# Kernel optimization log

Measured on AMD Instinct MI355X. Metric: run time of the kernel, lower is better.

Reference implementation:

```python
import jax, jax.numpy as jnp
import numpy as np

CUTOFF = 4.0
RBF_N = 32          # distance_embedding_size == D_rbf
F_DIM = 128         # hidden_size
N_ATOMS = 20000
N_PROBES = 100000
N_EDGES = 262144
LN_EPS = 1e-5


def setup_inputs() -> dict:
    key = jax.random.key(0)
    ks = jax.random.split(key, 20)
    s = 0.02
    inp = {
        "diff_pi": jax.random.normal(ks[0], (N_EDGES, 3), jnp.float32),
        "S_JK": jax.random.normal(ks[1], (N_ATOMS, F_DIM), jnp.float32),
        "V_JK": jax.random.normal(ks[2], (N_ATOMS, 3, F_DIM), jnp.float32),
        "atom_idx": jax.random.randint(ks[3], (N_EDGES,), 0, N_ATOMS),
        "probe_idx": jax.random.randint(ks[4], (N_EDGES,), 0, N_PROBES),
        "num_probes": N_PROBES,
        # state branch params
        "w_s1": jax.random.normal(ks[5], (3 * F_DIM, F_DIM), jnp.float32) * s,
        "b_s1": jnp.zeros((F_DIM,), jnp.float32),
        "g_ln": jnp.ones((F_DIM,), jnp.float32),
        "b_ln": jnp.zeros((F_DIM,), jnp.float32),
        "w_s2": jax.random.normal(ks[6], (F_DIM, F_DIM), jnp.float32) * s,
        "b_s2": jnp.zeros((F_DIM,), jnp.float32),
        # filter branch params
        "w_f1": jax.random.normal(ks[7], (RBF_N, F_DIM), jnp.float32) * s,
        "b_f1": jnp.zeros((F_DIM,), jnp.float32),
        "w_f2": jax.random.normal(ks[8], (F_DIM, F_DIM), jnp.float32) * s,
        "b_f2": jnp.zeros((F_DIM,), jnp.float32),
        # output head params
        "w_o1": jax.random.normal(ks[9], (F_DIM, F_DIM // 2), jnp.float32) * s,
        "b_o1": jnp.zeros((F_DIM // 2,), jnp.float32),
        "w_o2": jax.random.normal(ks[10], (F_DIM // 2, 1), jnp.float32) * s,
        "b_o2": jnp.zeros((1,), jnp.float32),
        "final_bias": jnp.array([-6.1], jnp.float32),
    }
    return inp


def reference(diff_pi, S_JK, V_JK, atom_idx, probe_idx, num_probes,
              w_s1, b_s1, g_ln, b_ln, w_s2, b_s2,
              w_f1, b_f1, w_f2, b_f2,
              w_o1, b_o1, w_o2, b_o2, final_bias):
    silu = jax.nn.silu
    # edge distances
    sq = (diff_pi ** 2).sum(-1)                       # [E]
    dist = jnp.sqrt(sq)                               # [E] exact distance
    dist_safe = jnp.sqrt(sq + 1e-8)[:, None]          # [E,1]
    r_hat = diff_pi / dist_safe                       # [E,3]

    # sinc RBF expansion: sin(n*pi*d/cutoff)/d, n=1..RBF_N
    n = jnp.arange(1, RBF_N + 1, dtype=diff_pi.dtype) # [D]
    e_pi = jnp.sin(dist[:, None] * n * (jnp.pi / CUTOFF)) / dist[:, None]  # [E,D]

    # gather atom features to edges
    n_i = jnp.sqrt((V_JK ** 2).sum(1) + 1e-8)         # [N,F]
    n_e = n_i[atom_idx]                               # [E,F]
    V_e = V_JK[atom_idx]                              # [E,3,F]
    q_pi = (V_e * r_hat[:, :, None]).sum(1)           # [E,F]
    S_e = S_JK[atom_idx]                              # [E,F]

    # state branch: Linear -> LayerNorm -> SiLU -> Linear
    h = jnp.concatenate([S_e, n_e, q_pi], axis=-1)    # [E,3F]
    u = h @ w_s1 + b_s1                               # [E,F]
    mu = u.mean(-1, keepdims=True)
    var = ((u - mu) ** 2).mean(-1, keepdims=True)
    u_norm = (u - mu) / jnp.sqrt(var + LN_EPS) * g_ln + b_ln
    state = silu(u_norm) @ w_s2 + b_s2                # [E,F]

    # filter branch (no normalization -> absolute distance scale)
    W = silu(e_pi @ w_f1 + b_f1) @ w_f2 + b_f2        # [E,F]

    # fuse + output head
    m = (silu((W * state) @ w_o1 + b_o1) @ w_o2 + b_o2)[:, 0]  # [E]

    x = dist / CUTOFF
    env = 1.0 - 21.0 * x ** 5 + 35.0 * x ** 6 - 15.0 * x ** 7
    env = jnp.where(dist < CUTOFF, env, jnp.zeros_like(env))
    m_w = m * env

    # scatter-add to probes
    rho = jax.ops.segment_sum(m_w, probe_idx, num_segments=num_probes)
    return rho + final_bias[0]
```

## Files before the change

kernel.cpp:

```cpp
#include <hip/hip_runtime.h>

#define EPB     64
#define E_TOTAL 262144
#define NPROBE  100000
#define N_ATOMS 20000
#define NTAB    2048

#define ASTR   136
#define A2_O   0
#define LDS_SH 8704

#define WS1_O  0
#define WS2_O  49152
#define WO1_O  65536
#define WT_TOT 73728
#define PQ_B   147456
#define WTI_B  20627456
#define WTF_B  21676032
#define CNT_B  22725120
#define CUR_B  22805120
#define SA_B   22885120
#define ED_B   23933696

typedef __attribute__((ext_vector_type(8))) short          short8;
typedef __attribute__((ext_vector_type(8))) unsigned short ushort8;
typedef __attribute__((ext_vector_type(4))) float          floatx4;

#define MFMA16(a, b, c) __builtin_amdgcn_mfma_f32_16x16x32_bf16((a), (b), (c), 0, 0, 0)

__device__ __forceinline__ unsigned short f2bfu(float x) {
    unsigned u = __builtin_bit_cast(unsigned, x);
    u = (u + 0x7FFFu + ((u >> 16) & 1u)) >> 16;
    return (unsigned short)u;
}
__device__ __forceinline__ unsigned pk2(float lo, float hi) {
    return __builtin_amdgcn_perm(__builtin_bit_cast(unsigned, hi),
                                 __builtin_bit_cast(unsigned, lo), 0x07060302u);
}
__device__ __forceinline__ float bf2f(unsigned short u) {
    return __builtin_bit_cast(float, ((unsigned)u) << 16);
}
__device__ __forceinline__ float silu_f(float x) { return x / (1.0f + __expf(-x)); }

struct F8 { float v[8]; };
__device__ __forceinline__ F8 ld8(const float* __restrict__ p) {
    F8 r;
    const float4 a = *(const float4*)p;
    const float4 b = *(const float4*)(p + 4);
    r.v[0] = a.x; r.v[1] = a.y; r.v[2] = a.z; r.v[3] = a.w;
    r.v[4] = b.x; r.v[5] = b.y; r.v[6] = b.z; r.v[7] = b.w;
    return r;
}

__global__ void cfr_prep_w(const float* __restrict__ w_s1, const float* __restrict__ w_s2,
                           const float* __restrict__ w_o1,
                           const float* __restrict__ fb, float* __restrict__ out,
                           unsigned short* __restrict__ wt, int* __restrict__ cnt) {
    int i = blockIdx.x * 256 + threadIdx.x;
    if (i < NPROBE) out[i] = fb[0];
    if (i < N_ATOMS) cnt[i] = 0;
    if (i < WT_TOT) {
        float v;
        if (i < WS2_O)      { int n = i / 384, k = i - n * 384;          v = w_s1[k * 128 + n]; }
        else if (i < WO1_O) { int j = i - WS2_O, n = j >> 7, k = j & 127; v = w_s2[k * 128 + n]; }
        else                { int j = i - WO1_O, n = j >> 7, k = j & 127; v = w_o1[k * 64 + n]; }
        wt[i] = f2bfu(v);
    }
}

__global__ void cfr_hist(const int* __restrict__ atom_idx, int* __restrict__ cnt) {
    int e = blockIdx.x * 256 + threadIdx.x;
    if (e < E_TOTAL) atomicAdd(&cnt[atom_idx[e]], 1);
}

__global__ __launch_bounds__(1024) void cfr_scan(const int* __restrict__ cnt,
                                                 int* __restrict__ cur) {
    __shared__ int part[1024];
    const int t = threadIdx.x, base = t * 20;
    int loc[20]; int s = 0;
#pragma unroll
    for (int i = 0; i < 20; ++i) {
        int v = (base + i < N_ATOMS) ? cnt[base + i] : 0;
        loc[i] = s; s += v;
    }
    part[t] = s;
    __syncthreads();
    for (int d = 1; d < 1024; d <<= 1) {
        int v = (t >= d) ? part[t - d] : 0;
        __syncthreads();
        part[t] += v;
        __syncthreads();
    }
    int pre = (t == 0) ? 0 : part[t - 1];
#pragma unroll
    for (int i = 0; i < 20; ++i)
        if (base + i < N_ATOMS) cur[base + i] = pre + loc[i];
}

__global__ void cfr_scatter(const int* __restrict__ atom_idx, const int* __restrict__ probe_idx,
                            const float* __restrict__ diff,
                            int* __restrict__ cur, int* __restrict__ sortedA,
                            float4* __restrict__ ediff) {
    int e = blockIdx.x * 256 + threadIdx.x;
    if (e >= E_TOTAL) return;
    int a = atom_idx[e];
    int pos = atomicAdd(&cur[a], 1);
    sortedA[pos] = a;
    float4 ed;
    ed.x = diff[e * 3 + 0]; ed.y = diff[e * 3 + 1]; ed.z = diff[e * 3 + 2];
    ed.w = __int_as_float(probe_idx[e]);
    ediff[pos] = ed;
}

__global__ __launch_bounds__(128) void cfr_prep_wtab(
    const float* __restrict__ w_f1, const float* __restrict__ b_f1,
    const float* __restrict__ w_f2, const float* __restrict__ b_f2,
    float* __restrict__ wtabF)
{
    __shared__ float ep[32];
    __shared__ float f1s[128];
    const int t = threadIdx.x, row = blockIdx.x;
    float d = fmaxf(row * (4.0f / NTAB), 1e-4f);
    if (t < 32) ep[t] = sinf(d * (t + 1) * 0.7853981633974483f) / d;
    __syncthreads();
    float f1 = b_f1[t];
#pragma unroll
    for (int k = 0; k < 32; ++k) f1 = fmaf(ep[k], w_f1[k * 128 + t], f1);
    f1s[t] = silu_f(f1);
    __syncthreads();
    float w = b_f2[t];
#pragma unroll 4
    for (int k = 0; k < 128; ++k) w = fmaf(f1s[k], w_f2[k * 128 + t], w);
    wtabF[row * 128 + t] = w;
}

__global__ void cfr_prep_wtab_pack(const float* __restrict__ wtabF,
                                   unsigned* __restrict__ wtabI) {
    int i = blockIdx.x * 256 + threadIdx.x;
    if (i >= NTAB * 128) return;
    int r = i >> 7, c = i & 127;
    unsigned lo = f2bfu(wtabF[r * 128 + c]);
    unsigned hi = f2bfu(wtabF[(r + 1) * 128 + c]);
    wtabI[i] = (hi << 16) | lo;
}

__global__ __launch_bounds__(256, 3) void cfr_prep_pq(
    const float* __restrict__ S, const float* __restrict__ V,
    const float* __restrict__ b_s1,
    const unsigned short* __restrict__ wt, unsigned short* __restrict__ pq)
{
    __shared__ __align__(16) unsigned short bufH[32 * 264];
    __shared__ __align__(16) unsigned short bufV[96 * 136];

    const int t    = threadIdx.x;
    const int a0   = blockIdx.x * 32;
    const int wave = t >> 6;
    const int lane = t & 63;
    const int q    = lane >> 4;
    const int c16  = lane & 15;

#pragma unroll
    for (int it = 0; it < 2; ++it) {
        int idx = it * 256 + t;
        int al = idx >> 4, f8 = (idx & 15) * 8;
        int a = a0 + al;
        ushort8 sS, sN, s0, s1, s2;
        if (a < N_ATOMS) {
            F8 s  = ld8(S + a * 128 + f8);
            F8 v0 = ld8(V + a * 384 + f8);
            F8 v1 = ld8(V + a * 384 + 128 + f8);
            F8 v2 = ld8(V + a * 384 + 256 + f8);
#pragma unroll
            for (int j = 0; j < 8; ++j) {
                sS[j] = f2bfu(s.v[j]);
                sN[j] = f2bfu(sqrtf(v0.v[j]*v0.v[j] + v1.v[j]*v1.v[j] + v2.v[j]*v2.v[j] + 1e-8f));
                s0[j] = f2bfu(v0.v[j]);
                s1[j] = f2bfu(v1.v[j]);
                s2[j] = f2bfu(v2.v[j]);
            }
        } else {
#pragma unroll
            for (int j = 0; j < 8; ++j) { sS[j]=0; sN[j]=0; s0[j]=0; s1[j]=0; s2[j]=0; }
        }
        *(ushort8*)&bufH[al * 264 + f8]        = sS;
        *(ushort8*)&bufH[al * 264 + 128 + f8]  = sN;
        *(ushort8*)&bufV[al * 136 + f8]        = s0;
        *(ushort8*)&bufV[(32 + al) * 136 + f8] = s1;
        *(ushort8*)&bufV[(64 + al) * 136 + f8] = s2;
    }
    __syncthreads();

    const floatx4 zero4 = {0.f, 0.f, 0.f, 0.f};
    float bs1c[2];
#pragma unroll
    for (int ni = 0; ni < 2; ++ni) bs1c[ni] = b_s1[wave * 32 + ni * 16 + c16];

    {
        floatx4 pacc[2][2];
#pragma unroll
        for (int mi = 0; mi < 2; ++mi) { pacc[mi][0] = zero4; pacc[mi][1] = zero4; }
#pragma unroll
        for (int kk = 0; kk < 8; ++kk) {
            short8 bfr[2], af[2];
#pragma unroll
            for (int ni = 0; ni < 2; ++ni) {
                int n = wave * 32 + ni * 16 + c16;
                bfr[ni] = *(const short8*)&wt[WS1_O + n * 384 + kk * 32 + q * 8];
            }
#pragma unroll
            for (int mi = 0; mi < 2; ++mi)
                af[mi] = *(const short8*)&bufH[(mi * 16 + c16) * 264 + kk * 32 + q * 8];
#pragma unroll
            for (int mi = 0; mi < 2; ++mi)
#pragma unroll
                for (int ni = 0; ni < 2; ++ni)
                    pacc[mi][ni] = MFMA16(af[mi], bfr[ni], pacc[mi][ni]);
        }
#pragma unroll
        for (int mi = 0; mi < 2; ++mi)
#pragma unroll
            for (int r = 0; r < 4; ++r) {
                int a = a0 + mi * 16 + q * 4 + r;
                if (a < N_ATOMS)
#pragma unroll
                    for (int ni = 0; ni < 2; ++ni) {
                        int col = wave * 32 + ni * 16 + c16;
                        pq[a * 512 + col] = f2bfu(pacc[mi][ni][r] + bs1c[ni]);
                    }
            }
    }

    short8 bq[4][2];
#pragma unroll
    for (int kk = 0; kk < 4; ++kk)
#pragma unroll
        for (int ni = 0; ni < 2; ++ni) {
            int n = wave * 32 + ni * 16 + c16;
            bq[kk][ni] = *(const short8*)&wt[WS1_O + n * 384 + 256 + kk * 32 + q * 8];
        }
#pragma unroll
    for (int d = 0; d < 3; ++d) {
        floatx4 qacc[2][2];
#pragma unroll
        for (int mi = 0; mi < 2; ++mi) { qacc[mi][0] = zero4; qacc[mi][1] = zero4; }
#pragma unroll
        for (int kk = 0; kk < 4; ++kk) {
            short8 af[2];
#pragma unroll
            for (int mi = 0; mi < 2; ++mi)
                af[mi] = *(const short8*)&bufV[(d * 32 + mi * 16 + c16) * 136 + kk * 32 + q * 8];
#pragma unroll
            for (int mi = 0; mi < 2; ++mi)
#pragma unroll
                for (int ni = 0; ni < 2; ++ni)
                    qacc[mi][ni] = MFMA16(af[mi], bq[kk][ni], qacc[mi][ni]);
        }
#pragma unroll
        for (int mi = 0; mi < 2; ++mi)
#pragma unroll
            for (int r = 0; r < 4; ++r) {
                int a = a0 + mi * 16 + q * 4 + r;
                if (a < N_ATOMS)
#pragma unroll
                    for (int ni = 0; ni < 2; ++ni) {
                        int col = wave * 32 + ni * 16 + c16;
                        pq[a * 512 + (1 + d) * 128 + col] = f2bfu(qacc[mi][ni][r]);
                    }
            }
    }
}

__global__ __launch_bounds__(256, 8) void cfr_main(
    const int* __restrict__ aidx, const float4* __restrict__ ediff,
    const unsigned short* __restrict__ wt, const unsigned short* __restrict__ pq,
    const unsigned* __restrict__ wtabI,
    const float* __restrict__ g_ln, const float* __restrict__ b_ln,
    const float* __restrict__ b_s2, const float* __restrict__ b_o1,
    const float* __restrict__ w_o2, const float* __restrict__ b_o2,
    float* __restrict__ out)
{
    __shared__ __align__(16) unsigned short LDSu[LDS_SH];
    __shared__ float df[EPB];
    __shared__ int   probe_s[EPB];
    __shared__ float mpart[EPB * 4];

    const int t    = threadIdx.x;
    const int e0   = blockIdx.x * EPB;
    const int wave = t >> 6;
    const int lane = t & 63;
    const int q    = lane >> 4;
    const int c16  = lane & 15;
    const floatx4 zero4 = {0.f, 0.f, 0.f, 0.f};

    const int el = t >> 2;
    const int c0 = (t & 3) * 32;

    {
        const int eg = e0 + el;
        const int a  = aidx[eg];
        float4 ed = ediff[eg];
        float sq = ed.x * ed.x + ed.y * ed.y + ed.z * ed.z;
        float dist = sqrtf(sq);
        float rinv = rsqrtf(sq + 1e-8f);
        float rx = ed.x * rinv, ry = ed.y * rinv, rz = ed.z * rinv;
        if ((t & 3) == 0) { df[el] = dist; probe_s[el] = __float_as_int(ed.w); }

        const ushort8* pqr = (const ushort8*)(pq + a * 512 + c0);
        float u[32];
#pragma unroll
        for (int g = 0; g < 4; ++g) {
            ushort8 v = pqr[g];
#pragma unroll
            for (int j = 0; j < 8; ++j) u[g * 8 + j] = bf2f(v[j]);
        }
#pragma unroll
        for (int g = 0; g < 4; ++g) {
            ushort8 v = pqr[16 + g];
#pragma unroll
            for (int j = 0; j < 8; ++j) u[g * 8 + j] = fmaf(bf2f(v[j]), rx, u[g * 8 + j]);
        }
#pragma unroll
        for (int g = 0; g < 4; ++g) {
            ushort8 v = pqr[32 + g];
#pragma unroll
            for (int j = 0; j < 8; ++j) u[g * 8 + j] = fmaf(bf2f(v[j]), ry, u[g * 8 + j]);
        }
#pragma unroll
        for (int g = 0; g < 4; ++g) {
            ushort8 v = pqr[48 + g];
#pragma unroll
            for (int j = 0; j < 8; ++j) u[g * 8 + j] = fmaf(bf2f(v[j]), rz, u[g * 8 + j]);
        }
        float s = 0.f, s2 = 0.f;
#pragma unroll
        for (int j = 0; j < 32; ++j) { s += u[j]; s2 = fmaf(u[j], u[j], s2); }
        s  += __shfl_xor(s, 1);  s  += __shfl_xor(s, 2);
        s2 += __shfl_xor(s2, 1); s2 += __shfl_xor(s2, 2);
        float mu = s * (1.f / 128.f);
        float rstd = rsqrtf(s2 * (1.f / 128.f) - mu * mu + 1e-5f);
        const float4* gp = (const float4*)(g_ln + c0);
        const float4* bp = (const float4*)(b_ln + c0);
        unsigned pko[16];
#pragma unroll
        for (int g4 = 0; g4 < 8; ++g4) {
            float4 gg = gp[g4], bb = bp[g4];
            float y0 = silu_f((u[g4 * 4 + 0] - mu) * rstd * gg.x + bb.x);
            float y1 = silu_f((u[g4 * 4 + 1] - mu) * rstd * gg.y + bb.y);
            float y2 = silu_f((u[g4 * 4 + 2] - mu) * rstd * gg.z + bb.z);
            float y3 = silu_f((u[g4 * 4 + 3] - mu) * rstd * gg.w + bb.w);
            pko[g4 * 2 + 0] = pk2(y0, y1);
            pko[g4 * 2 + 1] = pk2(y2, y3);
        }
        uint4* dst = (uint4*)&LDSu[A2_O + el * ASTR + c0];
        dst[0] = make_uint4(pko[0], pko[1], pko[2], pko[3]);
        dst[1] = make_uint4(pko[4], pko[5], pko[6], pko[7]);
        dst[2] = make_uint4(pko[8], pko[9], pko[10], pko[11]);
        dst[3] = make_uint4(pko[12], pko[13], pko[14], pko[15]);
    }
    __syncthreads();

    {
        floatx4 sacc[4][2];
#pragma unroll
        for (int mi = 0; mi < 4; ++mi) { sacc[mi][0] = zero4; sacc[mi][1] = zero4; }
#pragma unroll
        for (int kk = 0; kk < 4; ++kk) {
            short8 a2f[4], b2[2];
#pragma unroll
            for (int ni = 0; ni < 2; ++ni) {
                int n = wave * 32 + ni * 16 + c16;
                b2[ni] = *(const short8*)&wt[WS2_O + n * 128 + kk * 32 + q * 8];
            }
#pragma unroll
            for (int mi = 0; mi < 4; ++mi)
                a2f[mi] = *(const short8*)&LDSu[A2_O + (mi * 16 + c16) * ASTR + kk * 32 + q * 8];
#pragma unroll
            for (int mi = 0; mi < 4; ++mi)
#pragma unroll
                for (int ni = 0; ni < 2; ++ni)
                    sacc[mi][ni] = MFMA16(a2f[mi], b2[ni], sacc[mi][ni]);
        }
        __syncthreads();

        float bs2c[2];
#pragma unroll
        for (int ni = 0; ni < 2; ++ni) bs2c[ni] = b_s2[wave * 32 + ni * 16 + c16];
#pragma unroll
        for (int mi = 0; mi < 4; ++mi) {
#pragma unroll
            for (int r = 0; r < 4; ++r) {
                int row = mi * 16 + q * 4 + r;
                float f  = fminf(df[row] * (NTAB / 4.0f), NTAB - 1.01f);
                float fi = floorf(f);
                int   i0 = (int)fi;
                float fr = f - fi;
                const unsigned* wrow = wtabI + i0 * 128;
#pragma unroll
                for (int ni = 0; ni < 2; ++ni) {
                    int col = wave * 32 + ni * 16 + c16;
                    unsigned wp = wrow[col];
                    float w0 = __builtin_bit_cast(float, wp << 16);
                    float w1 = __builtin_bit_cast(float, wp & 0xffff0000u);
                    float wv = fmaf(fr, w1 - w0, w0);
                    float g  = (sacc[mi][ni][r] + bs2c[ni]) * wv;
                    LDSu[A2_O + row * ASTR + col] =
                        (unsigned short)(__builtin_bit_cast(unsigned, g) >> 16);
                }
            }
        }
    }
    __syncthreads();

    {
        const int n2 = wave * 16 + c16;
        floatx4 oacc[4];
#pragma unroll
        for (int mi = 0; mi < 4; ++mi) oacc[mi] = zero4;
#pragma unroll
        for (int kk = 0; kk < 4; ++kk) {
            short8 bfr = *(const short8*)&wt[WO1_O + n2 * 128 + kk * 32 + q * 8];
#pragma unroll
            for (int mi = 0; mi < 4; ++mi) {
                short8 af = *(const short8*)&LDSu[A2_O + (mi * 16 + c16) * ASTR + kk * 32 + q * 8];
                oacc[mi] = MFMA16(af, bfr, oacc[mi]);
            }
        }
        float bo1c = b_o1[n2], wo2c = w_o2[n2];
#pragma unroll
        for (int mi = 0; mi < 4; ++mi)
#pragma unroll
            for (int r = 0; r < 4; ++r) {
                float s = silu_f(oacc[mi][r] + bo1c) * wo2c;
#pragma unroll
                for (int d = 1; d < 16; d <<= 1) s += __shfl_xor(s, d, 64);
                if (c16 == 0) mpart[(mi * 16 + q * 4 + r) * 4 + wave] = s;
            }
    }
    __syncthreads();

    if (t < EPB) {
        float m = mpart[t * 4 + 0] + mpart[t * 4 + 1] + mpart[t * 4 + 2] + mpart[t * 4 + 3] + b_o2[0];
        float dd = df[t];
        float x  = dd * 0.25f;
        float x2 = x * x, x4 = x2 * x2;
        float x5 = x4 * x, x6 = x5 * x, x7 = x6 * x;
        float env = 1.0f - 21.0f * x5 + 35.0f * x6 - 15.0f * x7;
        env = (dd < 4.0f) ? env : 0.0f;
        float mw = m * env;
        if (mw != 0.f) unsafeAtomicAdd(&out[probe_s[t]], mw);
    }
}

extern "C" void kernel_launch(void* const* d_in, const int* in_sizes, int n_in,
                              void* d_out, int out_size, void* d_ws, size_t ws_size,
                              hipStream_t stream) {
    const float* diff    = (const float*)d_in[0];
    const float* S_JK    = (const float*)d_in[1];
    const float* V_JK    = (const float*)d_in[2];
    const int*   atom_i  = (const int*)d_in[3];
    const int*   probe_i = (const int*)d_in[4];
    const float* w_s1 = (const float*)d_in[6];
    const float* b_s1 = (const float*)d_in[7];
    const float* g_ln = (const float*)d_in[8];
    const float* b_ln = (const float*)d_in[9];
    const float* w_s2 = (const float*)d_in[10];
    const float* b_s2 = (const float*)d_in[11];
    const float* w_f1 = (const float*)d_in[12];
    const float* b_f1 = (const float*)d_in[13];
    const float* w_f2 = (const float*)d_in[14];
    const float* b_f2 = (const float*)d_in[15];
    const float* w_o1 = (const float*)d_in[16];
    const float* b_o1 = (const float*)d_in[17];
    const float* w_o2 = (const float*)d_in[18];
    const float* b_o2 = (const float*)d_in[19];
    const float* fbias = (const float*)d_in[20];
    float* out = (float*)d_out;

    char* ws = (char*)d_ws;
    unsigned short* wt    = (unsigned short*)ws;
    unsigned short* pqp   = (unsigned short*)(ws + PQ_B);
    unsigned*       wtabI = (unsigned*)(ws + WTI_B);
    float*          wtabF = (float*)(ws + WTF_B);
    int*            cnt   = (int*)(ws + CNT_B);
    int*            cur   = (int*)(ws + CUR_B);
    int*            srtA  = (int*)(ws + SA_B);
    float4*         edif  = (float4*)(ws + ED_B);

    cfr_prep_w<<<(NPROBE + 255) / 256, 256, 0, stream>>>(w_s1, w_s2, w_o1, fbias, out, wt, cnt);
    cfr_hist<<<E_TOTAL / 256, 256, 0, stream>>>(atom_i, cnt);
    cfr_scan<<<1, 1024, 0, stream>>>(cnt, cur);
    cfr_scatter<<<E_TOTAL / 256, 256, 0, stream>>>(atom_i, probe_i, diff, cur, srtA, edif);
    cfr_prep_wtab<<<NTAB + 1, 128, 0, stream>>>(w_f1, b_f1, w_f2, b_f2, wtabF);
    cfr_prep_wtab_pack<<<(NTAB * 128) / 256, 256, 0, stream>>>(wtabF, wtabI);
    cfr_prep_pq<<<(N_ATOMS + 31) / 32, 256, 0, stream>>>(S_JK, V_JK, b_s1, wt, pqp);
    cfr_main<<<E_TOTAL / EPB, 256, 0, stream>>>(srtA, edif, wt, pqp, wtabI,
        g_ln, b_ln, b_s2, b_o1, w_o2, b_o2, out);
}
```

Before: 290.1 us.

## Merge preprocessing kernels into fewer launches and pack atom index into edge record

Folds the output init, weight transpose, histogram and filter-table build into one launch. The scan now runs as block 0 of the atom projection kernel, and the table build computes adjacent row pairs directly, without a float staging buffer or a separate pack pass. The atom index is packed into the high bits of the probe-index word of the sorted edge record, which drops the sortedA array and one load stream in the main kernel. Together this removes four launches and some memory traffic, at the cost of a serial 79-element-per-thread scan in a single block and a 17-bit limit on probe indices.

```diff
diff --git a/kernel.cpp b/kernel.cpp
--- a/kernel.cpp
+++ b/kernel.cpp
@@ -16,11 +16,14 @@
 #define WT_TOT 73728
 #define PQ_B   147456
 #define WTI_B  20627456
-#define WTF_B  21676032
-#define CNT_B  22725120
-#define CUR_B  22805120
-#define SA_B   22885120
-#define ED_B   23933696
+#define CNT_B  21676032
+#define CUR_B  21756032
+#define ED_B   21836032
+
+#define L_WT_OFF   NPROBE
+#define L_HIST_OFF (NPROBE + WT_TOT)
+#define L_TOT      (L_HIST_OFF + E_TOTAL)
+#define LINB       ((L_TOT + 255) / 256)
 
 typedef __attribute__((ext_vector_type(8))) short          short8;
 typedef __attribute__((ext_vector_type(8))) unsigned short ushort8;
@@ -52,108 +55,94 @@
     return r;
 }
 
-__global__ void cfr_prep_w(const float* __restrict__ w_s1, const float* __restrict__ w_s2,
-                           const float* __restrict__ w_o1,
-                           const float* __restrict__ fb, float* __restrict__ out,
-                           unsigned short* __restrict__ wt, int* __restrict__ cnt) {
-    int i = blockIdx.x * 256 + threadIdx.x;
-    if (i < NPROBE) out[i] = fb[0];
-    if (i < N_ATOMS) cnt[i] = 0;
-    if (i < WT_TOT) {
-        float v;
-        if (i < WS2_O)      { int n = i / 384, k = i - n * 384;          v = w_s1[k * 128 + n]; }
-        else if (i < WO1_O) { int j = i - WS2_O, n = j >> 7, k = j & 127; v = w_s2[k * 128 + n]; }
-        else                { int j = i - WO1_O, n = j >> 7, k = j & 127; v = w_o1[k * 64 + n]; }
-        wt[i] = f2bfu(v);
-    }
-}
-
-__global__ void cfr_hist(const int* __restrict__ atom_idx, int* __restrict__ cnt) {
-    int e = blockIdx.x * 256 + threadIdx.x;
-    if (e < E_TOTAL) atomicAdd(&cnt[atom_idx[e]], 1);
-}
-
-__global__ __launch_bounds__(1024) void cfr_scan(const int* __restrict__ cnt,
-                                                 int* __restrict__ cur) {
-    __shared__ int part[1024];
-    const int t = threadIdx.x, base = t * 20;
-    int loc[20]; int s = 0;
-#pragma unroll
-    for (int i = 0; i < 20; ++i) {
-        int v = (base + i < N_ATOMS) ? cnt[base + i] : 0;
-        loc[i] = s; s += v;
-    }
-    part[t] = s;
-    __syncthreads();
-    for (int d = 1; d < 1024; d <<= 1) {
-        int v = (t >= d) ? part[t - d] : 0;
-        __syncthreads();
-        part[t] += v;
-        __syncthreads();
-    }
-    int pre = (t == 0) ? 0 : part[t - 1];
-#pragma unroll
-    for (int i = 0; i < 20; ++i)
-        if (base + i < N_ATOMS) cur[base + i] = pre + loc[i];
-}
-
-__global__ void cfr_scatter(const int* __restrict__ atom_idx, const int* __restrict__ probe_idx,
-                            const float* __restrict__ diff,
-                            int* __restrict__ cur, int* __restrict__ sortedA,
-                            float4* __restrict__ ediff) {
-    int e = blockIdx.x * 256 + threadIdx.x;
-    if (e >= E_TOTAL) return;
-    int a = atom_idx[e];
-    int pos = atomicAdd(&cur[a], 1);
-    sortedA[pos] = a;
-    float4 ed;
-    ed.x = diff[e * 3 + 0]; ed.y = diff[e * 3 + 1]; ed.z = diff[e * 3 + 2];
-    ed.w = __int_as_float(probe_idx[e]);
-    ediff[pos] = ed;
-}
-
-__global__ __launch_bounds__(128) void cfr_prep_wtab(
+__global__ __launch_bounds__(256) void cfr_prep1(
+    const float* __restrict__ w_s1, const float* __restrict__ w_s2,
+    const float* __restrict__ w_o1,
     const float* __restrict__ w_f1, const float* __restrict__ b_f1,
     const float* __restrict__ w_f2, const float* __restrict__ b_f2,
-    float* __restrict__ wtabF)
+    const int* __restrict__ atom_idx,
+    const float* __restrict__ fb, float* __restrict__ out,
+    unsigned short* __restrict__ wt, int* __restrict__ cnt,
+    unsigned* __restrict__ wtabI)
 {
-    __shared__ float ep[32];
-    __shared__ float f1s[128];
-    const int t = threadIdx.x, row = blockIdx.x;
-    float d = fmaxf(row * (4.0f / NTAB), 1e-4f);
-    if (t < 32) ep[t] = sinf(d * (t + 1) * 0.7853981633974483f) / d;
-    __syncthreads();
-    float f1 = b_f1[t];
-#pragma unroll
-    for (int k = 0; k < 32; ++k) f1 = fmaf(ep[k], w_f1[k * 128 + t], f1);
-    f1s[t] = silu_f(f1);
-    __syncthreads();
-    float w = b_f2[t];
+    __shared__ float ep[2][32];
+    __shared__ float f1s[2][128];
+    __shared__ float ws[2][128];
+    const int t = threadIdx.x;
+
+    if (blockIdx.x < LINB) {
+        int i = blockIdx.x * 256 + t;
+        if (i < NPROBE) {
+            out[i] = fb[0];
+        } else if (i < L_HIST_OFF) {
+            int j = i - L_WT_OFF;
+            float v;
+            if (j < WS2_O)      { int n = j / 384, k = j - n * 384;           v = w_s1[k * 128 + n]; }
+            else if (j < WO1_O) { int m = j - WS2_O, n = m >> 7, k = m & 127; v = w_s2[k * 128 + n]; }
+            else                { int m = j - WO1_O, n = m >> 7, k = m & 127; v = w_o1[k * 64 + n]; }
+            wt[j] = f2bfu(v);
+        } else if (i < L_TOT) {
+            atomicAdd(&cnt[atom_idx[i - L_HIST_OFF]], 1);
+        }
+        return;
+    }
+
+    const int r    = blockIdx.x - LINB;
+    const int half = t >> 7;
+    const int c    = t & 127;
+    float d = fmaxf((r + half) * (4.0f / NTAB), 1e-4f);
+    if (c < 32) ep[half][c] = sinf(d * (c + 1) * 0.7853981633974483f) / d;
+    __syncthreads();
+    float f1 = b_f1[c];
+#pragma unroll
+    for (int k = 0; k < 32; ++k) f1 = fmaf(ep[half][k], w_f1[k * 128 + c], f1);
+    f1s[half][c] = silu_f(f1);
+    __syncthreads();
+    float w = b_f2[c];
 #pragma unroll 4
-    for (int k = 0; k < 128; ++k) w = fmaf(f1s[k], w_f2[k * 128 + t], w);
-    wtabF[row * 128 + t] = w;
-}
-
-__global__ void cfr_prep_wtab_pack(const float* __restrict__ wtabF,
-                                   unsigned* __restrict__ wtabI) {
-    int i = blockIdx.x * 256 + threadIdx.x;
-    if (i >= NTAB * 128) return;
-    int r = i >> 7, c = i & 127;
-    unsigned lo = f2bfu(wtabF[r * 128 + c]);
-    unsigned hi = f2bfu(wtabF[(r + 1) * 128 + c]);
-    wtabI[i] = (hi << 16) | lo;
-}
-
-__global__ __launch_bounds__(256, 3) void cfr_prep_pq(
+    for (int k = 0; k < 128; ++k) w = fmaf(f1s[half][k], w_f2[k * 128 + c], w);
+    ws[half][c] = w;
+    __syncthreads();
+    if (half == 0)
+        wtabI[r * 128 + c] = ((unsigned)f2bfu(ws[1][c]) << 16) | (unsigned)f2bfu(ws[0][c]);
+}
+
+__global__ __launch_bounds__(256, 3) void cfr_prep2(
     const float* __restrict__ S, const float* __restrict__ V,
     const float* __restrict__ b_s1,
-    const unsigned short* __restrict__ wt, unsigned short* __restrict__ pq)
+    const unsigned short* __restrict__ wt, unsigned short* __restrict__ pq,
+    const int* __restrict__ cnt, int* __restrict__ cur)
 {
-    __shared__ __align__(16) unsigned short bufH[32 * 264];
-    __shared__ __align__(16) unsigned short bufV[96 * 136];
-
-    const int t    = threadIdx.x;
-    const int a0   = blockIdx.x * 32;
+    __shared__ __align__(16) unsigned short lds[21504];
+    unsigned short* bufH = lds;
+    unsigned short* bufV = lds + 8448;
+    const int t = threadIdx.x;
+
+    if (blockIdx.x == 0) {
+        int* part = (int*)lds;
+        const int base = t * 79;
+        int loc[79]; int s = 0;
+#pragma unroll 1
+        for (int i = 0; i < 79; ++i) {
+            int v = (base + i < N_ATOMS) ? cnt[base + i] : 0;
+            loc[i] = s; s += v;
+        }
+        part[t] = s;
+        __syncthreads();
+        for (int d = 1; d < 256; d <<= 1) {
+            int v = (t >= d) ? part[t - d] : 0;
+            __syncthreads();
+            part[t] += v;
+            __syncthreads();
+        }
+        int pre = (t == 0) ? 0 : part[t - 1];
+#pragma unroll 1
+        for (int i = 0; i < 79; ++i)
+            if (base + i < N_ATOMS) cur[base + i] = pre + loc[i];
+        return;
+    }
+
+    const int a0   = (blockIdx.x - 1) * 32;
     const int wave = t >> 6;
     const int lane = t & 63;
     const int q    = lane >> 4;
@@ -270,8 +259,21 @@
     }
 }
 
+__global__ void cfr_scatter(const int* __restrict__ atom_idx, const int* __restrict__ probe_idx,
+                            const float* __restrict__ diff,
+                            int* __restrict__ cur, float4* __restrict__ ediff) {
+    int e = blockIdx.x * 256 + threadIdx.x;
+    if (e >= E_TOTAL) return;
+    int a = atom_idx[e];
+    int pos = atomicAdd(&cur[a], 1);
+    float4 ed;
+    ed.x = diff[e * 3 + 0]; ed.y = diff[e * 3 + 1]; ed.z = diff[e * 3 + 2];
+    ed.w = __uint_as_float(((unsigned)a << 17) | (unsigned)probe_idx[e]);
+    ediff[pos] = ed;
+}
+
 __global__ __launch_bounds__(256, 8) void cfr_main(
-    const int* __restrict__ aidx, const float4* __restrict__ ediff,
+    const float4* __restrict__ ediff,
     const unsigned short* __restrict__ wt, const unsigned short* __restrict__ pq,
     const unsigned* __restrict__ wtabI,
     const float* __restrict__ g_ln, const float* __restrict__ b_ln,
@@ -296,14 +298,14 @@
     const int c0 = (t & 3) * 32;
 
     {
-        const int eg = e0 + el;
-        const int a  = aidx[eg];
-        float4 ed = ediff[eg];
+        float4 ed = ediff[e0 + el];
+        unsigned key = __float_as_uint(ed.w);
+        const int a = (int)(key >> 17);
         float sq = ed.x * ed.x + ed.y * ed.y + ed.z * ed.z;
         float dist = sqrtf(sq);
         float rinv = rsqrtf(sq + 1e-8f);
         float rx = ed.x * rinv, ry = ed.y * rinv, rz = ed.z * rinv;
-        if ((t & 3) == 0) { df[el] = dist; probe_s[el] = __float_as_int(ed.w); }
+        if ((t & 3) == 0) { df[el] = dist; probe_s[el] = (int)(key & 0x1FFFFu); }
 
         const ushort8* pqr = (const ushort8*)(pq + a * 512 + c0);
         float u[32];
@@ -480,19 +482,15 @@
     unsigned short* wt    = (unsigned short*)ws;
     unsigned short* pqp   = (unsigned short*)(ws + PQ_B);
     unsigned*       wtabI = (unsigned*)(ws + WTI_B);
-    float*          wtabF = (float*)(ws + WTF_B);
     int*            cnt   = (int*)(ws + CNT_B);
     int*            cur   = (int*)(ws + CUR_B);
-    int*            srtA  = (int*)(ws + SA_B);
     float4*         edif  = (float4*)(ws + ED_B);
 
-    cfr_prep_w<<<(NPROBE + 255) / 256, 256, 0, stream>>>(w_s1, w_s2, w_o1, fbias, out, wt, cnt);
-    cfr_hist<<<E_TOTAL / 256, 256, 0, stream>>>(atom_i, cnt);
-    cfr_scan<<<1, 1024, 0, stream>>>(cnt, cur);
-    cfr_scatter<<<E_TOTAL / 256, 256, 0, stream>>>(atom_i, probe_i, diff, cur, srtA, edif);
-    cfr_prep_wtab<<<NTAB + 1, 128, 0, stream>>>(w_f1, b_f1, w_f2, b_f2, wtabF);
-    cfr_prep_wtab_pack<<<(NTAB * 128) / 256, 256, 0, stream>>>(wtabF, wtabI);
-    cfr_prep_pq<<<(N_ATOMS + 31) / 32, 256, 0, stream>>>(S_JK, V_JK, b_s1, wt, pqp);
-    cfr_main<<<E_TOTAL / EPB, 256, 0, stream>>>(srtA, edif, wt, pqp, wtabI,
+    hipMemsetAsync(cnt, 0, N_ATOMS * sizeof(int), stream);
+    cfr_prep1<<<LINB + NTAB, 256, 0, stream>>>(w_s1, w_s2, w_o1, w_f1, b_f1, w_f2, b_f2,
+                                               atom_i, fbias, out, wt, cnt, wtabI);
+    cfr_prep2<<<1 + (N_ATOMS + 31) / 32, 256, 0, stream>>>(S_JK, V_JK, b_s1, wt, pqp, cnt, cur);
+    cfr_scatter<<<E_TOTAL / 256, 256, 0, stream>>>(atom_i, probe_i, diff, cur, edif);
+    cfr_main<<<E_TOTAL / EPB, 256, 0, stream>>>(edif, wt, pqp, wtabI,
         g_ln, b_ln, b_s2, b_o1, w_o2, b_o2, out);
 }
```

Result: slower. 307.5 us (+6.0%).
